# Kernel tuning notes

Measured on AMD Instinct MI355X. Metric: run time of the kernel, lower is better.

Reference implementation:

```python
import jax, jax.numpy as jnp
import numpy as np

P = 256          # planes == in_planes
EPS = 1e-5       # BatchNorm eps


def binarize(x):
    # sign with sign(0) -> +1, as in standard binary-net quantizers
    return jnp.where(x >= 0, 1.0, -1.0).astype(x.dtype)


def bin_conv(x, w, stride=1):
    """XNOR-style binarized 3x3 conv: sign(x) * sign(w), scaled by per-out-channel mean |w|."""
    ba = binarize(x)
    bw = binarize(w)
    scale = jnp.mean(jnp.abs(w), axis=(1, 2, 3))  # [O]
    y = jax.lax.conv_general_dilated(
        ba, bw, window_strides=(stride, stride), padding=((1, 1), (1, 1)),
        dimension_numbers=("NCHW", "OIHW", "NCHW"))
    return y * scale[None, :, None, None]


def bn(x, gamma, beta, mean, var):
    # inference-mode BatchNorm2d
    inv = gamma / jnp.sqrt(var + EPS)
    return x * inv[None, :, None, None] + (beta - mean * inv)[None, :, None, None]


def channel_shuffle(x, groups=2):
    b, c, h, w = x.shape
    return x.reshape(b, groups, c // groups, h, w).transpose(0, 2, 1, 3, 4).reshape(b, c, h, w)


def setup_inputs() -> dict:
    key = jax.random.key(0)
    ks = jax.random.split(key, 8)
    B, H, W = 16, 56, 56
    return {
        "x": jax.random.normal(ks[0], (B, 2 * P, H, W), jnp.float32),
        "w1": jax.random.normal(ks[1], (P, P, 3, 3), jnp.float32) * 0.05,
        "w2": jax.random.normal(ks[2], (P, 2 * P, 3, 3), jnp.float32) * 0.05,
        "gamma1": jnp.ones((P,), jnp.float32),
        "beta1": jnp.zeros((P,), jnp.float32),
        "mean1": jax.random.normal(ks[3], (P,), jnp.float32) * 0.1,
        "var1": jax.random.uniform(ks[4], (P,), jnp.float32) + 0.5,
        "gamma2": jnp.ones((P,), jnp.float32),
        "beta2": jnp.zeros((P,), jnp.float32),
        "mean2": jax.random.normal(ks[5], (P,), jnp.float32) * 0.1,
        "var2": jax.random.uniform(ks[6], (P,), jnp.float32) + 0.5,
        "move_bias": jax.random.normal(ks[7], (1, P, 1, 1), jnp.float32) * 0.1,
    }


def reference(x, w1, w2, gamma1, beta1, mean1, var1,
              gamma2, beta2, mean2, var2, move_bias):
    x_act, x_idle = x[:, :P], x[:, P:]
    residual = x_act
    out = bn(bin_conv(x_act, w1, stride=1), gamma1, beta1, mean1, var1)
    out = out + residual
    out = jnp.clip(out, -1.0, 1.0)            # Hardtanh
    x_idle = x_idle + move_bias               # LearnableBias
    out = jnp.concatenate([out, x_idle], axis=1)   # [B, 2P, H, W]
    out = channel_shuffle(out, groups=2)
    residual1 = out[:, :P]
    out = bn(bin_conv(out, w2, stride=1), gamma2, beta2, mean2, var2)
    out = out + residual1
    out = jnp.clip(out, -1.0, 1.0)            # Hardtanh
    return out
```

## Files before the change

kernel.cpp:

```cpp
#include <hip/hip_runtime.h>
#include <cstdint>

typedef unsigned long long u64;
typedef unsigned short u16;

#define HWSZ 3136
#define WD 56
#define NPIX 50176
#define HS 58
#define IMG 3364

__device__ __forceinline__ float clampf(float v){ return fminf(1.0f, fmaxf(-1.0f, v)); }
__device__ __forceinline__ u16 f2bf(float f){
    unsigned u = __float_as_uint(f);
    return (u16)((u + 0x7fffu + ((u >> 16) & 1u)) >> 16);
}
__device__ __forceinline__ float bf2f(u16 h){ return __uint_as_float(((unsigned)h) << 16); }
__device__ __forceinline__ int xp(u64 a, u64 b, int s){
    u64 x = a ^ b;
    s += __popc((unsigned)x);
    s += __popc((unsigned)(x >> 32));
    return s;
}

__device__ __forceinline__ void conv_pass(
    const u64* __restrict__ bits, const u64* __restrict__ wsrc, int colbase,
    int base, int (&accA)[8][2], int (&accB)[8][2])
{
#pragma unroll 1
    for (int dy = -1; dy <= 1; dy++) {
        const ulonglong2* rp = (const ulonglong2*)(bits + (size_t)(base + dy * HS) * 4);
        ulonglong2 plo[4], phi[4];
#pragma unroll
        for (int k = 0; k < 4; k++) { plo[k] = rp[2 * k]; phi[k] = rp[2 * k + 1]; }
        int tb = (dy + 1) * 3;
#pragma unroll
        for (int dx = 0; dx < 3; dx++) {
#pragma unroll
            for (int co = 0; co < 8; co++) {
                const u64* wp = wsrc + ((size_t)(colbase + co) * 9 + tb + dx) * 4;
                u64 wa0 = wp[0], wa1 = wp[1], wb0 = wp[2], wb1 = wp[3];
#pragma unroll
                for (int p = 0; p < 2; p++) {
                    int k = dx + p; int s = accA[co][p];
                    s = xp(plo[k].x, wa0, s); s = xp(plo[k].y, wa1, s);
                    s = xp(phi[k].x, wb0, s); s = xp(phi[k].y, wb1, s);
                    accA[co][p] = s;
                }
            }
#pragma unroll
            for (int co = 0; co < 8; co++) {
                const u64* wp = wsrc + ((size_t)(colbase + 8 + co) * 9 + tb + dx) * 4;
                u64 wa0 = wp[0], wa1 = wp[1], wb0 = wp[2], wb1 = wp[3];
#pragma unroll
                for (int p = 0; p < 2; p++) {
                    int k = dx + p; int s = accB[co][p];
                    s = xp(plo[k].x, wa0, s); s = xp(plo[k].y, wa1, s);
                    s = xp(phi[k].x, wb0, s); s = xp(phi[k].y, wb1, s);
                    accB[co][p] = s;
                }
            }
        }
    }
}

__global__ __launch_bounds__(256) void k_wprep(
    const float* __restrict__ w1, const float* __restrict__ w2,
    const float* __restrict__ g1, const float* __restrict__ be1,
    const float* __restrict__ m1, const float* __restrict__ v1,
    const float* __restrict__ g2, const float* __restrict__ be2,
    const float* __restrict__ m2, const float* __restrict__ v2,
    u64* __restrict__ w1b, u64* __restrict__ w2e, u64* __restrict__ w2o,
    float* __restrict__ A1, float* __restrict__ B1,
    float* __restrict__ A2, float* __restrict__ B2,
    int* __restrict__ C1s, int* __restrict__ C2s)
{
    int co  = blockIdx.x;
    int tid = threadIdx.x;
    int wv = tid >> 6, lane = tid & 63;
    int ci = (wv << 6) + lane;

    __shared__ int spc1[4][9], spc2[4][9];

    float s1 = 0.f, s2 = 0.f;
    const float* w1p = w1 + ((size_t)co * 256 + ci) * 9;
#pragma unroll
    for (int t = 0; t < 9; t++) {
        float v = w1p[t];
        s1 += fabsf(v);
        u64 bal = __ballot(v >= 0.f);
        if (lane == 0) { w1b[(co * 9 + t) * 4 + wv] = bal; spc1[wv][t] = __popcll(bal); }
    }
    const float* wep = w2 + ((size_t)co * 512 + 2 * ci) * 9;
    const float* wop = wep + 9;
#pragma unroll
    for (int t = 0; t < 9; t++) {
        float ve = wep[t], vo = wop[t];
        s2 += fabsf(ve) + fabsf(vo);
        u64 bale = __ballot(ve >= 0.f);
        u64 balo = __ballot(vo >= 0.f);
        if (lane == 0) {
            w2e[(co * 9 + t) * 4 + wv] = bale; w2o[(co * 9 + t) * 4 + wv] = balo;
            spc2[wv][t] = __popcll(bale) + __popcll(balo);
        }
    }
    __shared__ float red1[256], red2[256];
    red1[tid] = s1; red2[tid] = s2;
    __syncthreads();
    for (int off = 128; off > 0; off >>= 1) {
        if (tid < off) { red1[tid] += red1[tid + off]; red2[tid] += red2[tid + off]; }
        __syncthreads();
    }
    if (tid == 0) {
        float scale1 = red1[0] / 2304.f;
        float scale2 = red2[0] / 4608.f;
        float inv1 = g1[co] / sqrtf(v1[co] + 1e-5f);
        float inv2 = g2[co] / sqrtf(v2[co] + 1e-5f);
        A1[co] = scale1 * inv1;  B1[co] = be1[co] - m1[co] * inv1;
        A2[co] = scale2 * inv2;  B2[co] = be2[co] - m2[co] * inv2;
        int pc1[9], pc2[9];
#pragma unroll
        for (int t = 0; t < 9; t++) {
            pc1[t] = spc1[0][t] + spc1[1][t] + spc1[2][t] + spc1[3][t];
            pc2[t] = spc2[0][t] + spc2[1][t] + spc2[2][t] + spc2[3][t];
        }
        int* c1 = C1s + co * 8;
        c1[0] = pc1[0] + pc1[1] + pc1[2];
        c1[1] = pc1[6] + pc1[7] + pc1[8];
        c1[2] = pc1[0] + pc1[3] + pc1[6];
        c1[3] = pc1[2] + pc1[5] + pc1[8];
        c1[4] = pc1[0]; c1[5] = pc1[2]; c1[6] = pc1[6]; c1[7] = pc1[8];
        int* c2 = C2s + co * 8;
        c2[0] = pc2[0] + pc2[1] + pc2[2];
        c2[1] = pc2[6] + pc2[7] + pc2[8];
        c2[2] = pc2[0] + pc2[3] + pc2[6];
        c2[3] = pc2[2] + pc2[5] + pc2[8];
        c2[4] = pc2[0]; c2[5] = pc2[2]; c2[6] = pc2[6]; c2[7] = pc2[8];
    }
}

__global__ __launch_bounds__(256) void k_zero(ulonglong2* __restrict__ dst, int n)
{
    int i = blockIdx.x * 256 + threadIdx.x;
    if (i < n) { ulonglong2 z; z.x = 0; z.y = 0; dst[i] = z; }
}

__global__ __launch_bounds__(256) void k_pack(
    const float* __restrict__ x, const float* __restrict__ mb,
    u64* __restrict__ bitsA, u64* __restrict__ bitsI)
{
    int tid = threadIdx.x;
    int p = blockIdx.x * 256 + tid;
    int q = blockIdx.y;
    int b = p / HWSZ, hw = p % HWSZ;
    int h = hw / WD, w = hw % WD;
    const float* xa = x + ((size_t)(b * 512 + q * 64)) * HWSZ + hw;
    const float* xi = x + ((size_t)(b * 512 + 256 + q * 64)) * HWSZ + hw;
    const float* mbq = mb + q * 64;
    u64 wa = 0, wi = 0;
#pragma unroll 8
    for (int j = 0; j < 64; j++) {
        float va = xa[(size_t)j * HWSZ];
        float vi = xi[(size_t)j * HWSZ] + mbq[j];
        wa |= (u64)(va >= 0.f) << j;
        wi |= (u64)(vi >= 0.f) << j;
    }
    size_t pos = ((size_t)b * IMG + (h + 1) * HS + (w + 1)) * 4 + q;
    bitsA[pos] = wa;
    bitsI[pos] = wi;
}

__global__ __launch_bounds__(512, 6) void k_conv1(
    const float* __restrict__ x, const u64* __restrict__ bitsA,
    const u64* __restrict__ w1b, const float* __restrict__ A1,
    const float* __restrict__ B1, const int* __restrict__ C1s,
    u64* __restrict__ bitsC, u16* __restrict__ c1v)
{
    __shared__ float sA[64], sB[64];
    __shared__ int scr[512];
    __shared__ u16 spart[4][256];
    int tid = threadIdx.x, q = blockIdx.y, cobase = q * 64;
    if (tid < 64) { sA[tid] = A1[cobase + tid]; sB[tid] = B1[cobase + tid]; }
    scr[tid] = C1s[cobase * 8 + tid];
    __syncthreads();

    int wid = tid >> 6, lane = tid & 63;
    int gu = __builtin_amdgcn_readfirstlane(wid & 3);
    int ph = wid >> 2;
    int pix0 = blockIdx.x * 256 + ph * 128 + lane * 2;
    int b = pix0 / HWSZ, hw = pix0 % HWSZ, h = hw / WD, w = hw % WD;
    int base = b * IMG + (h + 1) * HS + w;

    int accA[8][2] = {}, accB[8][2] = {};
    conv_pass(bitsA, w1b, cobase + (gu << 4), base, accA, accB);

    int mt = (h == 0), mbo = (h == WD - 1);
    int wl = (w == 0), wr = (w == 54);
    int nvr = 3 - mt - mbo;
    int nv0 = nvr * (3 - wl), nv1 = nvr * (3 - wr);

    unsigned sb0 = 0, sb1 = 0;
    bool wrv = (q < 2);
#pragma unroll
    for (int half = 0; half < 2; half++)
#pragma unroll
    for (int co = 0; co < 8; co++) {
        int col = (gu << 4) + half * 8 + co;
        int coG = cobase + col, bit = half * 8 + co;
        float A = sA[col], Bc = sB[col];
        const int* cs = &scr[col * 8];
        int a0 = half ? accB[co][0] : accA[co][0];
        int a1 = half ? accB[co][1] : accA[co][1];
        int ctb = (mt ? cs[0] : 0) + (mbo ? cs[1] : 0);
        int corr0 = ctb + (wl ? (cs[2] - (mt ? cs[4] : 0) - (mbo ? cs[6] : 0)) : 0);
        int corr1 = ctb + (wr ? (cs[3] - (mt ? cs[5] : 0) - (mbo ? cs[7] : 0)) : 0);
        float2 xr = *(const float2*)(x + ((size_t)(b * 512 + coG)) * HWSZ + hw);
        float v0 = (float)((nv0 << 8) + 2 * (corr0 - a0)) * A + Bc + xr.x;
        float v1 = (float)((nv1 << 8) + 2 * (corr1 - a1)) * A + Bc + xr.y;
        sb0 |= (unsigned)(v0 >= 0.f) << bit;
        sb1 |= (unsigned)(v1 >= 0.f) << bit;
        if (wrv) {
            ushort2 st; st.x = f2bf(clampf(v0)); st.y = f2bf(clampf(v1));
            *(ushort2*)(c1v + (size_t)coG * NPIX + pix0) = st;
        }
    }
    spart[gu][ph * 128 + lane * 2]     = (u16)sb0;
    spart[gu][ph * 128 + lane * 2 + 1] = (u16)sb1;
    __syncthreads();
    if ((wid & 3) == 0) {
#pragma unroll
        for (int p = 0; p < 2; p++) {
            int pi = ph * 128 + lane * 2 + p;
            u64 word = (u64)spart[0][pi] | ((u64)spart[1][pi] << 16)
                     | ((u64)spart[2][pi] << 32) | ((u64)spart[3][pi] << 48);
            bitsC[(size_t)(base + 1 + p) * 4 + q] = word;
        }
    }
}

__global__ __launch_bounds__(512, 6) void k_conv2(
    const float* __restrict__ x, const float* __restrict__ mb,
    const u64* __restrict__ bitsC, const u64* __restrict__ bitsI,
    const u64* __restrict__ w2e, const u64* __restrict__ w2o,
    const float* __restrict__ A2, const float* __restrict__ B2,
    const int* __restrict__ C2s,
    const u16* __restrict__ c1v, float* __restrict__ out)
{
    __shared__ __align__(16) u64 se[2304], so[2304];
    __shared__ float sA[64], sB[64], sM[32];
    __shared__ int scr[512];
    int tid = threadIdx.x, q = blockIdx.y, cobase = q * 64;
    {
        const u64* srcE = w2e + (size_t)cobase * 36;
        const u64* srcO = w2o + (size_t)cobase * 36;
        for (int i = tid; i < 2304; i += 512) { se[i] = srcE[i]; so[i] = srcO[i]; }
        if (tid < 64) { sA[tid] = A2[cobase + tid]; sB[tid] = B2[cobase + tid]; }
        if (tid >= 64 && tid < 96) sM[tid - 64] = mb[q * 32 + tid - 64];
        scr[tid] = C2s[cobase * 8 + tid];
    }
    __syncthreads();

    int wid = tid >> 6, lane = tid & 63;
    int gu = __builtin_amdgcn_readfirstlane(wid & 3);
    int ph = wid >> 2;
    int pix0 = blockIdx.x * 256 + ph * 128 + lane * 2;
    int b = pix0 / HWSZ, hw = pix0 % HWSZ, h = hw / WD, w = hw % WD;
    int base = b * IMG + (h + 1) * HS + w;

    int accA[8][2] = {}, accB[8][2] = {};
    conv_pass(bitsC, se, gu << 4, base, accA, accB);
    conv_pass(bitsI, so, gu << 4, base, accA, accB);

    int mt = (h == 0), mbo = (h == WD - 1);
    int wl = (w == 0), wr = (w == 54);
    int nvr = 3 - mt - mbo;
    int nv0 = nvr * (3 - wl), nv1 = nvr * (3 - wr);

#pragma unroll
    for (int half = 0; half < 2; half++)
#pragma unroll
    for (int co = 0; co < 8; co++) {
        int col = (gu << 4) + half * 8 + co;
        int coG = cobase + col, cg2 = coG >> 1;
        float A = sA[col], Bc = sB[col];
        const int* cs = &scr[col * 8];
        int a0 = half ? accB[co][0] : accA[co][0];
        int a1 = half ? accB[co][1] : accA[co][1];
        int ctb = (mt ? cs[0] : 0) + (mbo ? cs[1] : 0);
        int corr0 = ctb + (wl ? (cs[2] - (mt ? cs[4] : 0) - (mbo ? cs[6] : 0)) : 0);
        int corr1 = ctb + (wr ? (cs[3] - (mt ? cs[5] : 0) - (mbo ? cs[7] : 0)) : 0);
        float r0, r1;
        if ((co & 1) == 0) {
            ushort2 cv = *(const ushort2*)(c1v + (size_t)cg2 * NPIX + pix0);
            r0 = bf2f(cv.x); r1 = bf2f(cv.y);
        } else {
            float2 xi = *(const float2*)(x + ((size_t)(b * 512 + 256 + cg2)) * HWSZ + hw);
            float mv = sM[col >> 1];
            r0 = xi.x + mv; r1 = xi.y + mv;
        }
        float2 ov;
        ov.x = clampf((float)((nv0 << 9) + 2 * (corr0 - a0)) * A + Bc + r0);
        ov.y = clampf((float)((nv1 << 9) + 2 * (corr1 - a1)) * A + Bc + r1);
        *(float2*)(out + ((size_t)(b * 256 + coG)) * HWSZ + hw) = ov;
    }
}

extern "C" void kernel_launch(void* const* d_in, const int* in_sizes, int n_in,
                              void* d_out, int out_size, void* d_ws, size_t ws_size,
                              hipStream_t stream)
{
    const float* x   = (const float*)d_in[0];
    const float* w1  = (const float*)d_in[1];
    const float* w2  = (const float*)d_in[2];
    const float* g1  = (const float*)d_in[3];
    const float* be1 = (const float*)d_in[4];
    const float* m1  = (const float*)d_in[5];
    const float* v1  = (const float*)d_in[6];
    const float* g2  = (const float*)d_in[7];
    const float* be2 = (const float*)d_in[8];
    const float* m2  = (const float*)d_in[9];
    const float* v2  = (const float*)d_in[10];
    const float* mb  = (const float*)d_in[11];

    char* ws = (char*)d_ws;
    u64* w1b = (u64*)ws; ws += 73728;
    u64* w2e = (u64*)ws; ws += 73728;
    u64* w2o = (u64*)ws; ws += 73728;
    float* A1 = (float*)ws; ws += 1024;
    float* B1 = (float*)ws; ws += 1024;
    float* A2 = (float*)ws; ws += 1024;
    float* B2 = (float*)ws; ws += 1024;
    int* C1s = (int*)ws; ws += 8192;
    int* C2s = (int*)ws; ws += 8192;
    u64* bitsA = (u64*)ws; ws += (size_t)16 * IMG * 4 * 8;
    u64* bitsI = (u64*)ws; ws += (size_t)16 * IMG * 4 * 8;
    u64* bitsC = (u64*)ws; ws += (size_t)16 * IMG * 4 * 8;
    u16* c1v = (u16*)ws; ws += (size_t)128 * NPIX * 2;

    int nzero2 = (int)(3 * (size_t)16 * IMG * 4 * 8 / 16);

    hipLaunchKernelGGL(k_wprep, dim3(256), dim3(256), 0, stream,
                       w1, w2, g1, be1, m1, v1, g2, be2, m2, v2,
                       w1b, w2e, w2o, A1, B1, A2, B2, C1s, C2s);
    hipLaunchKernelGGL(k_zero, dim3((nzero2 + 255) / 256), dim3(256), 0, stream,
                       (ulonglong2*)bitsA, nzero2);
    hipLaunchKernelGGL(k_pack, dim3(196, 4), dim3(256), 0, stream, x, mb, bitsA, bitsI);
    hipLaunchKernelGGL(k_conv1, dim3(196, 4), dim3(512), 0, stream,
                       x, bitsA, w1b, A1, B1, C1s, bitsC, c1v);
    hipLaunchKernelGGL(k_conv2, dim3(196, 4), dim3(512), 0, stream,
                       x, mb, bitsC, bitsI, w2e, w2o, A2, B2, C2s, c1v, (float*)d_out);
}
```

Baseline: 484.1 us.

## Stage conv1 weights in LDS and halve conv block size to 256 threads

conv1 now copies its 64-channel slice of binarized weights into shared memory, as conv2 already did, instead of reading them from global memory inside the inner loop. Both conv kernels switch from 512-thread blocks covering 256 pixels to 256-thread blocks covering 128 pixels, with the grid doubled. Weight reads are changed to 128-bit vector loads. Smaller blocks may improve scheduling flexibility, but the per-block weight staging is now repeated over twice as many blocks, and the new launch bounds change the register budget.

Measured after the change: 438.5 us. 9.4% less time.

```diff
diff --git a/kernel.cpp b/kernel.cpp
--- a/kernel.cpp
+++ b/kernel.cpp
@@ -23,8 +23,8 @@
     return s;
 }
 
-__device__ __forceinline__ void conv_pass(
-    const u64* __restrict__ bits, const u64* __restrict__ wsrc, int colbase,
+__device__ __forceinline__ void conv_pass2(
+    const u64* __restrict__ bits, const u64* wlds, int colbase,
     int base, int (&accA)[8][2], int (&accB)[8][2])
 {
 #pragma unroll 1
@@ -33,30 +33,30 @@
         ulonglong2 plo[4], phi[4];
 #pragma unroll
         for (int k = 0; k < 4; k++) { plo[k] = rp[2 * k]; phi[k] = rp[2 * k + 1]; }
-        int tb = (dy + 1) * 3;
 #pragma unroll
         for (int dx = 0; dx < 3; dx++) {
+            int t = (dy + 1) * 3 + dx;
 #pragma unroll
             for (int co = 0; co < 8; co++) {
-                const u64* wp = wsrc + ((size_t)(colbase + co) * 9 + tb + dx) * 4;
-                u64 wa0 = wp[0], wa1 = wp[1], wb0 = wp[2], wb1 = wp[3];
+                const ulonglong2* wp = (const ulonglong2*)&wlds[((colbase + co) * 9 + t) * 4];
+                ulonglong2 wA = wp[0], wB = wp[1];
 #pragma unroll
                 for (int p = 0; p < 2; p++) {
                     int k = dx + p; int s = accA[co][p];
-                    s = xp(plo[k].x, wa0, s); s = xp(plo[k].y, wa1, s);
-                    s = xp(phi[k].x, wb0, s); s = xp(phi[k].y, wb1, s);
+                    s = xp(plo[k].x, wA.x, s); s = xp(plo[k].y, wA.y, s);
+                    s = xp(phi[k].x, wB.x, s); s = xp(phi[k].y, wB.y, s);
                     accA[co][p] = s;
                 }
             }
 #pragma unroll
             for (int co = 0; co < 8; co++) {
-                const u64* wp = wsrc + ((size_t)(colbase + 8 + co) * 9 + tb + dx) * 4;
-                u64 wa0 = wp[0], wa1 = wp[1], wb0 = wp[2], wb1 = wp[3];
+                const ulonglong2* wp = (const ulonglong2*)&wlds[((colbase + 8 + co) * 9 + t) * 4];
+                ulonglong2 wA = wp[0], wB = wp[1];
 #pragma unroll
                 for (int p = 0; p < 2; p++) {
                     int k = dx + p; int s = accB[co][p];
-                    s = xp(plo[k].x, wa0, s); s = xp(plo[k].y, wa1, s);
-                    s = xp(phi[k].x, wb0, s); s = xp(phi[k].y, wb1, s);
+                    s = xp(plo[k].x, wA.x, s); s = xp(plo[k].y, wA.y, s);
+                    s = xp(phi[k].x, wB.x, s); s = xp(phi[k].y, wB.y, s);
                     accB[co][p] = s;
                 }
             }
@@ -170,29 +170,35 @@
     bitsI[pos] = wi;
 }
 
-__global__ __launch_bounds__(512, 6) void k_conv1(
+__global__ __launch_bounds__(256, 4) void k_conv1(
     const float* __restrict__ x, const u64* __restrict__ bitsA,
     const u64* __restrict__ w1b, const float* __restrict__ A1,
     const float* __restrict__ B1, const int* __restrict__ C1s,
     u64* __restrict__ bitsC, u16* __restrict__ c1v)
 {
+    __shared__ __align__(16) u64 sw[2304];
     __shared__ float sA[64], sB[64];
     __shared__ int scr[512];
-    __shared__ u16 spart[4][256];
+    __shared__ u16 spart[4][128];
     int tid = threadIdx.x, q = blockIdx.y, cobase = q * 64;
-    if (tid < 64) { sA[tid] = A1[cobase + tid]; sB[tid] = B1[cobase + tid]; }
-    scr[tid] = C1s[cobase * 8 + tid];
+    {
+        const u64* src = w1b + (size_t)cobase * 36;
+#pragma unroll
+        for (int i = 0; i < 9; i++) sw[tid + i * 256] = src[tid + i * 256];
+        if (tid < 64) { sA[tid] = A1[cobase + tid]; sB[tid] = B1[cobase + tid]; }
+        scr[tid] = C1s[cobase * 8 + tid];
+        scr[tid + 256] = C1s[cobase * 8 + tid + 256];
+    }
     __syncthreads();
 
     int wid = tid >> 6, lane = tid & 63;
-    int gu = __builtin_amdgcn_readfirstlane(wid & 3);
-    int ph = wid >> 2;
-    int pix0 = blockIdx.x * 256 + ph * 128 + lane * 2;
+    int gu = __builtin_amdgcn_readfirstlane(wid);
+    int pix0 = blockIdx.x * 128 + lane * 2;
     int b = pix0 / HWSZ, hw = pix0 % HWSZ, h = hw / WD, w = hw % WD;
     int base = b * IMG + (h + 1) * HS + w;
 
     int accA[8][2] = {}, accB[8][2] = {};
-    conv_pass(bitsA, w1b, cobase + (gu << 4), base, accA, accB);
+    conv_pass2(bitsA, sw, gu << 4, base, accA, accB);
 
     int mt = (h == 0), mbo = (h == WD - 1);
     int wl = (w == 0), wr = (w == 54);
@@ -224,13 +230,13 @@
             *(ushort2*)(c1v + (size_t)coG * NPIX + pix0) = st;
         }
     }
-    spart[gu][ph * 128 + lane * 2]     = (u16)sb0;
-    spart[gu][ph * 128 + lane * 2 + 1] = (u16)sb1;
+    spart[wid][lane * 2]     = (u16)sb0;
+    spart[wid][lane * 2 + 1] = (u16)sb1;
     __syncthreads();
-    if ((wid & 3) == 0) {
+    if (wid == 0) {
 #pragma unroll
         for (int p = 0; p < 2; p++) {
-            int pi = ph * 128 + lane * 2 + p;
+            int pi = lane * 2 + p;
             u64 word = (u64)spart[0][pi] | ((u64)spart[1][pi] << 16)
                      | ((u64)spart[2][pi] << 32) | ((u64)spart[3][pi] << 48);
             bitsC[(size_t)(base + 1 + p) * 4 + q] = word;
@@ -238,7 +244,7 @@
     }
 }
 
-__global__ __launch_bounds__(512, 6) void k_conv2(
+__global__ __launch_bounds__(256, 4) void k_conv2(
     const float* __restrict__ x, const float* __restrict__ mb,
     const u64* __restrict__ bitsC, const u64* __restrict__ bitsI,
     const u64* __restrict__ w2e, const u64* __restrict__ w2o,
@@ -253,23 +259,24 @@
     {
         const u64* srcE = w2e + (size_t)cobase * 36;
         const u64* srcO = w2o + (size_t)cobase * 36;
-        for (int i = tid; i < 2304; i += 512) { se[i] = srcE[i]; so[i] = srcO[i]; }
+#pragma unroll
+        for (int i = 0; i < 9; i++) { se[tid + i * 256] = srcE[tid + i * 256]; so[tid + i * 256] = srcO[tid + i * 256]; }
         if (tid < 64) { sA[tid] = A2[cobase + tid]; sB[tid] = B2[cobase + tid]; }
         if (tid >= 64 && tid < 96) sM[tid - 64] = mb[q * 32 + tid - 64];
         scr[tid] = C2s[cobase * 8 + tid];
+        scr[tid + 256] = C2s[cobase * 8 + tid + 256];
     }
     __syncthreads();
 
     int wid = tid >> 6, lane = tid & 63;
-    int gu = __builtin_amdgcn_readfirstlane(wid & 3);
-    int ph = wid >> 2;
-    int pix0 = blockIdx.x * 256 + ph * 128 + lane * 2;
+    int gu = __builtin_amdgcn_readfirstlane(wid);
+    int pix0 = blockIdx.x * 128 + lane * 2;
     int b = pix0 / HWSZ, hw = pix0 % HWSZ, h = hw / WD, w = hw % WD;
     int base = b * IMG + (h + 1) * HS + w;
 
     int accA[8][2] = {}, accB[8][2] = {};
-    conv_pass(bitsC, se, gu << 4, base, accA, accB);
-    conv_pass(bitsI, so, gu << 4, base, accA, accB);
+    conv_pass2(bitsC, se, gu << 4, base, accA, accB);
+    conv_pass2(bitsI, so, gu << 4, base, accA, accB);
 
     int mt = (h == 0), mbo = (h == WD - 1);
     int wl = (w == 0), wr = (w == 54);
@@ -345,8 +352,8 @@
     hipLaunchKernelGGL(k_zero, dim3((nzero2 + 255) / 256), dim3(256), 0, stream,
                        (ulonglong2*)bitsA, nzero2);
     hipLaunchKernelGGL(k_pack, dim3(196, 4), dim3(256), 0, stream, x, mb, bitsA, bitsI);
-    hipLaunchKernelGGL(k_conv1, dim3(196, 4), dim3(512), 0, stream,
+    hipLaunchKernelGGL(k_conv1, dim3(392, 4), dim3(256), 0, stream,
                        x, bitsA, w1b, A1, B1, C1s, bitsC, c1v);
-    hipLaunchKernelGGL(k_conv2, dim3(196, 4), dim3(512), 0, stream,
+    hipLaunchKernelGGL(k_conv2, dim3(392, 4), dim3(256), 0, stream,
                        x, mb, bitsC, bitsI, w2e, w2o, A2, B2, C2s, c1v, (float*)d_out);
 }
```
